# Kernel tuning notes

Hardware: AMD Instinct MI355X
Metric: run time of the kernel (lower is better)

## Reference

```python
import jax, jax.numpy as jnp
import numpy as np

EPS = 1e-5
K = 5          # kernel size from SE3Convolution(5, ...)
STRIDE = 2
PAD = 3
C_HID = 52     # 4*dim(repr3x3=9) + dim(repr7=7) + dim(repr9=9)
N_CLASSES = 10


def conv3d(x, w):
    # x: [N, Cin, D, H, W], w: [Cout, Cin, K, K, K]
    return jax.lax.conv_general_dilated(
        x, w,
        window_strides=(STRIDE, STRIDE, STRIDE),
        padding=[(PAD, PAD)] * 3,
        dimension_numbers=("NCDHW", "OIDHW", "NCDHW"),
    )


def bn3d(x):
    # training-mode batch norm over (batch, spatial), per channel, no affine
    mean = jnp.mean(x, axis=(0, 2, 3, 4), keepdims=True)
    var = jnp.var(x, axis=(0, 2, 3, 4), keepdims=True)
    return (x - mean) * jax.lax.rsqrt(var + EPS)


def setup_inputs() -> dict:
    key = jax.random.key(0)
    ks = jax.random.split(key, 10)
    x = jax.random.normal(ks[0], (32, 1, 64, 64, 64), dtype=jnp.float32)
    s = 0.05
    w0 = jax.random.normal(ks[1], (C_HID, 1, K, K, K), jnp.float32) * s
    b0 = jax.random.normal(ks[2], (C_HID,), jnp.float32) * s
    w1 = jax.random.normal(ks[3], (C_HID, C_HID, K, K, K), jnp.float32) * s
    b1 = jax.random.normal(ks[4], (C_HID,), jnp.float32) * s
    w2 = jax.random.normal(ks[5], (C_HID, C_HID, K, K, K), jnp.float32) * s
    b2 = jax.random.normal(ks[6], (C_HID,), jnp.float32) * s
    w3 = jax.random.normal(ks[7], (N_CLASSES, C_HID, K, K, K), jnp.float32) * s
    gamma = jnp.ones((N_CLASSES,), jnp.float32)
    beta = jnp.zeros((N_CLASSES,), jnp.float32)
    return {"x": x, "w0": w0, "b0": b0, "w1": w1, "b1": b1,
            "w2": w2, "b2": b2, "w3": w3, "gamma": gamma, "beta": beta}


def reference(x, w0, b0, w1, b1, w2, b2, w3, gamma, beta):
    # bn_in: BatchNorm3d(1, affine=False)
    h = bn3d(x)
    # three conv blocks with scalar batch norm + bias + ReLU (non_lin layers)
    for w, b in ((w0, b0), (w1, b1), (w2, b2)):
        h = conv3d(h, w)
        h = bn3d(h)
        h = jax.nn.relu(h + b[None, :, None, None, None])
    # final conv (no nonlinearity)
    h = conv3d(h, w3)
    # global average pool over x, y, z -> [batch, classes]
    h = jnp.mean(h, axis=(2, 3, 4))
    # bn_out: affine batch norm over the batch dim, per class
    mean = jnp.mean(h, axis=0, keepdims=True)
    var = jnp.var(h, axis=0, keepdims=True)
    h = (h - mean) * jax.lax.rsqrt(var + EPS)
    return h * gamma[None, :] + beta[None, :]
```

## Files before the change

kernel.cpp:

```cpp
#include <hip/hip_runtime.h>
#include <hip/hip_bf16.h>

#define EPSV 1e-5f
constexpr int NB = 32;

typedef short bf16x8 __attribute__((ext_vector_type(8)));
typedef short short4v __attribute__((ext_vector_type(4)));
typedef float f32x4 __attribute__((ext_vector_type(4)));

__device__ inline float bf2f(short s) {
  return __uint_as_float(((unsigned)(unsigned short)s) << 16);
}
__device__ inline short f2bf(float f) {
  unsigned u = __float_as_uint(f);
  unsigned r = (u + 0x7FFFu + ((u >> 16) & 1u)) >> 16;
  return (short)r;
}

__global__ __launch_bounds__(256) void reduce_partial_f32(
    const float* __restrict__ in, int spatial, float* __restrict__ part,
    int totb, int boff)
{
  const int b = blockIdx.x;
  const int nblk = gridDim.x;
  float s = 0.f, s2 = 0.f;
  for (int n = 0; n < NB; ++n) {
    const float* p = in + (size_t)n * spatial;
    for (int i = b * 256 + threadIdx.x; i < spatial; i += nblk * 256) {
      float v = p[i];
      s += v; s2 += v * v;
    }
  }
  __shared__ float sh[256], sh2[256];
  int tid = threadIdx.x;
  sh[tid] = s; sh2[tid] = s2;
  __syncthreads();
  for (int off = 128; off > 0; off >>= 1) {
    if (tid < off) { sh[tid] += sh[tid + off]; sh2[tid] += sh2[tid + off]; }
    __syncthreads();
  }
  if (tid == 0) {
    part[(size_t)(boff + b) * 2 + 0] = sh[0];
    part[(size_t)(boff + b) * 2 + 1] = sh2[0];
  }
}

__global__ __launch_bounds__(256) void reduce_cl(
    const short* __restrict__ y, long nrows,
    float* __restrict__ part, int totb, int boff)
{
  const int b = blockIdx.x, nblk = gridDim.x;
  const int c = threadIdx.x & 63, seg = threadIdx.x >> 6;
  float s = 0.f, s2 = 0.f;
  for (long r = (long)b * 4 + seg; r < nrows; r += (long)nblk * 4) {
    float v = bf2f(y[r * 64 + c]);
    s += v; s2 += v * v;
  }
  __shared__ float sh[4][64], sh2[4][64];
  sh[seg][c] = s; sh2[seg][c] = s2;
  __syncthreads();
  if (seg == 0) {
    float a = sh[0][c] + sh[1][c] + sh[2][c] + sh[3][c];
    float a2 = sh2[0][c] + sh2[1][c] + sh2[2][c] + sh2[3][c];
    part[((size_t)c * totb + boff + b) * 2 + 0] = a;
    part[((size_t)c * totb + boff + b) * 2 + 1] = a2;
  }
}

__global__ __launch_bounds__(64) void reduce_final(
    const float* __restrict__ part, int nblk, int C, float* __restrict__ sums)
{
  const int c = blockIdx.x;
  float s = 0.f, s2 = 0.f;
  for (int b = threadIdx.x; b < nblk; b += 64) {
    s  += part[((size_t)c * nblk + b) * 2 + 0];
    s2 += part[((size_t)c * nblk + b) * 2 + 1];
  }
  for (int off = 32; off > 0; off >>= 1) {
    s  += __shfl_down(s, off);
    s2 += __shfl_down(s2, off);
  }
  if (threadIdx.x == 0) { sums[c] = s; sums[C + c] = s2; }
}

__global__ __launch_bounds__(64) void aff_k(
    const float* __restrict__ st, const float* __restrict__ bias,
    float cnt_inv, int creal, float* __restrict__ a, float* __restrict__ c)
{
  int t = threadIdx.x;
  float mean = st[t] * cnt_inv;
  float var  = st[64 + t] * cnt_inv - mean * mean;
  float inv  = rsqrtf(var + EPSV);
  bool ok = t < creal;
  a[t] = ok ? inv : 0.f;
  c[t] = ok ? (-mean * inv + bias[t]) : 0.f;
}

__global__ __launch_bounds__(256) void repack_k(
    const float* __restrict__ w, short* __restrict__ wt,
    int CO, int CIN, int COP)
{
  long total = 125L * COP * 64;
  for (long idx = (long)blockIdx.x * 256 + threadIdx.x; idx < total;
       idx += (long)gridDim.x * 256) {
    int tap = (int)(idx / (COP * 64));
    int r   = (int)(idx % (COP * 64));
    int co = r >> 6, ci = r & 63;
    float v = (co < CO && ci < CIN) ? w[((size_t)co * CIN + ci) * 125 + tap] : 0.f;
    wt[idx] = f2bf(v);
  }
}

__global__ __launch_bounds__(256) void repack_w0(
    const float* __restrict__ w, short* __restrict__ wt)
{
  for (int idx = blockIdx.x * 256 + threadIdx.x; idx < 64 * 128;
       idx += gridDim.x * 256) {
    int co = idx >> 7, k = idx & 127;
    float v = (co < 52 && k < 125) ? w[co * 125 + k] : 0.f;
    wt[idx] = f2bf(v);
  }
}

__global__ __launch_bounds__(256) void conv0_mfma(
    const float* __restrict__ x, const short* __restrict__ w0t,
    const float* __restrict__ stats, short* __restrict__ out,
    int n_in0, int n_out0)
{
  constexpr int IN = 64, OUT = 33;
  constexpr float CNTI = 1.0f / ((float)NB * IN * IN * IN);
  __shared__ __align__(16) char slab[64 * 256];

  const int tid = threadIdx.x;
  const int wv = tid >> 6, ln = tid & 63;
  const int cs = ln >> 4;
  const int ntile0 = blockIdx.x * 64;
  const int od = blockIdx.y;
  const int img = blockIdx.z;

  const float mean = stats[0] * CNTI;
  const float inv  = rsqrtf(stats[1] * CNTI - mean * mean + EPSV);

  bf16x8 afr[4];
  {
    const short* wrow = w0t + (wv * 16 + (ln & 15)) * 128 + cs * 8;
    #pragma unroll
    for (int ks = 0; ks < 4; ++ks) afr[ks] = *(const bf16x8*)(wrow + ks * 32);
  }

  const float* xi = x + (size_t)(n_in0 + img) * (IN * IN * IN);
  const int id_base = 2 * od - 3;
  for (int u = tid; u < 1024; u += 256) {
    const int nl = u >> 4, s = u & 15;
    const int ng = ntile0 + nl;
    const int oh = ng / OUT, ow = ng - oh * OUT;
    const bool nok = ng < OUT * OUT;
    const int ih_base = 2 * oh - 3, iw_base = 2 * ow - 3;
    bf16x8 pk;
    #pragma unroll
    for (int e = 0; e < 8; ++e) {
      const int k = s * 8 + e;
      float f = 0.f;
      if (nok && k < 125) {
        const int kd = k / 25, r = k - kd * 25;
        const int kh = r / 5, kw = r - kh * 5;
        const int id = id_base + kd, ih = ih_base + kh, iw = iw_base + kw;
        if ((unsigned)id < (unsigned)IN && (unsigned)ih < (unsigned)IN &&
            (unsigned)iw < (unsigned)IN)
          f = (xi[((size_t)id * IN + ih) * IN + iw] - mean) * inv;
      }
      pk[e] = f2bf(f);
    }
    const int slot = (s & 8) | ((s & 7) ^ (nl & 7));
    *(bf16x8*)(slab + nl * 256 + slot * 16) = pk;
  }
  __syncthreads();

  const int nl = ln & 15;
  #pragma unroll
  for (int nt = 0; nt < 4; ++nt) {
    f32x4 acc = (f32x4){0.f, 0.f, 0.f, 0.f};
    const int nn = nt * 16 + nl;
    #pragma unroll
    for (int ks = 0; ks < 4; ++ks) {
      const int s = ks * 4 + cs;
      const int slot = (s & 8) | ((s & 7) ^ (nn & 7));
      bf16x8 b = *(const bf16x8*)(slab + nn * 256 + slot * 16);
      acc = __builtin_amdgcn_mfma_f32_16x16x32_bf16(afr[ks], b, acc, 0, 0, 0);
    }
    const int ng = ntile0 + nn;
    if (ng < OUT * OUT) {
      const int oh = ng / OUT, ow = ng - oh * OUT;
      short4v pk;
      #pragma unroll
      for (int r = 0; r < 4; ++r) pk[r] = f2bf(acc[r]);
      size_t base = ((((size_t)(n_out0 + img) * OUT + od) * OUT + oh) * OUT + ow) * 64;
      *(short4v*)(out + base + wv * 16 + cs * 4) = pk;
    }
  }
}

__device__ inline int swz(int lin, int cs) {
  int row = lin >> 1;
  int slot = (((lin & 1) << 2) | cs) ^ (row & 7);
  return row * 128 + slot * 16;
}

__device__ __forceinline__ void loada2(bf16x8 (&dst)[2][5], const short* __restrict__ wt,
                                       int tapb, int ch, int wm, int nl, int cs) {
  #pragma unroll
  for (int mi = 0; mi < 2; ++mi)
    #pragma unroll
    for (int kw = 0; kw < 5; ++kw)
      dst[mi][kw] = *(const bf16x8*)(
          wt + ((size_t)(tapb + kw) * 64 + (2 * wm + mi) * 16 + nl) * 64 + ch * 32 + cs * 8);
}

template<int IN, int OUT, int OHG>
__global__ __launch_bounds__(256, 2) void conv_2m2n(
    const short* __restrict__ yin, const short* __restrict__ wt,
    const float* __restrict__ affa, const float* __restrict__ affc,
    short* __restrict__ yout, int n_out0)
{
  constexpr int W = 2 * OUT + 3;
  constexpr int H = 2 * OHG + 3;
  constexpr int LIN = H * W;
  constexpr int ROWS = (LIN + 1) / 2;
  constexpr int OHT = (OUT + OHG - 1) / OHG;
  constexpr int LINM = LIN - 1 - 4 * W - 4;

  __shared__ __align__(16) char slab[ROWS * 128];
  __shared__ float s_a[64], s_c[64];

  const int tid = threadIdx.x;
  const int wv = tid >> 6, ln = tid & 63;
  const int nl = ln & 15, cs = ln >> 4;
  const int wm = wv >> 1, wn = wv & 1;

  int lin;
  if (gridDim.x & 7) lin = blockIdx.x;
  else {
    const int q = gridDim.x >> 3;
    lin = (blockIdx.x & 7) * q + (blockIdx.x >> 3);
  }
  const int oht = lin % OHT;
  const int t2  = lin / OHT;
  const int od  = t2 % OUT;
  const int nimg = t2 / OUT;
  const int oh0 = oht * OHG;

  if (tid < 64) { s_a[tid] = affa[tid]; s_c[tid] = affc[tid]; }

  int lb[2]; bool vld[2]; size_t obase[2];
  #pragma unroll
  for (int j = 0; j < 2; ++j) {
    int nt = 2 * wn + j;
    int n = nt * 16 + nl;
    int ohl = n / OUT, ow = n - ohl * OUT;
    vld[j] = n < OHG * OUT;
    int l = 2 * ohl * W + 2 * ow;
    lb[j] = (l > LINM) ? LINM : l;
    obase[j] = ((((size_t)(n_out0 + nimg) * OUT + od) * OUT + (oh0 + ohl)) * OUT + ow) * 64;
  }

  f32x4 acc[2][2];
  #pragma unroll
  for (int mi = 0; mi < 2; ++mi)
    #pragma unroll
    for (int j = 0; j < 2; ++j) acc[mi][j] = (f32x4){0.f, 0.f, 0.f, 0.f};

  const int id_base = 2 * od - 3;
  const int ih_base = 2 * oh0 - 3;

  for (int ch = 0; ch < 2; ++ch) {
    for (int kd = 0; kd < 5; ++kd) {
      __syncthreads();
      {
        const int id = id_base + kd;
        const bool dok = (unsigned)id < (unsigned)IN;
        for (int u = tid; u < LIN * 4; u += 256) {
          int l = u >> 2, cs2 = u & 3;
          int hl = l / W, wl = l - hl * W;
          int ih = ih_base + hl;
          int iw = wl - 3;
          bf16x8 pk;
          if (dok && (unsigned)ih < (unsigned)IN && (unsigned)iw < (unsigned)IN) {
            size_t base = ((((size_t)nimg * IN + id) * IN + ih) * IN + iw) * 64
                          + ch * 32 + cs2 * 8;
            bf16x8 ld = *(const bf16x8*)(yin + base);
            #pragma unroll
            for (int e = 0; e < 8; ++e) {
              int c = ch * 32 + cs2 * 8 + e;
              pk[e] = f2bf(fmaxf(s_a[c] * bf2f(ld[e]) + s_c[c], 0.f));
            }
          } else {
            #pragma unroll
            for (int e = 0; e < 8; ++e) pk[e] = 0;
          }
          *(bf16x8*)(slab + swz(l, cs2)) = pk;
        }
      }
      bf16x8 afr[2][2][5];
      loada2(afr[0], wt, (kd * 5 + 0) * 5, ch, wm, nl, cs);
      __builtin_amdgcn_sched_barrier(0);
      __syncthreads();
      #pragma unroll
      for (int kh = 0; kh < 5; ++kh) {
        if (kh < 4)
          loada2(afr[(kh + 1) & 1], wt, (kd * 5 + kh + 1) * 5, ch, wm, nl, cs);
        __builtin_amdgcn_sched_barrier(0);
        #pragma unroll
        for (int kw = 0; kw < 5; ++kw) {
          bf16x8 b0 = *(const bf16x8*)(slab + swz(lb[0] + kh * W + kw, cs));
          bf16x8 b1 = *(const bf16x8*)(slab + swz(lb[1] + kh * W + kw, cs));
          #pragma unroll
          for (int mi = 0; mi < 2; ++mi) {
            acc[mi][0] = __builtin_amdgcn_mfma_f32_16x16x32_bf16(
                afr[kh & 1][mi][kw], b0, acc[mi][0], 0, 0, 0);
            acc[mi][1] = __builtin_amdgcn_mfma_f32_16x16x32_bf16(
                afr[kh & 1][mi][kw], b1, acc[mi][1], 0, 0, 0);
          }
        }
      }
    }
  }

  #pragma unroll
  for (int j = 0; j < 2; ++j) {
    if (!vld[j]) continue;
    #pragma unroll
    for (int mi = 0; mi < 2; ++mi) {
      short4v pk;
      #pragma unroll
      for (int r = 0; r < 4; ++r) pk[r] = f2bf(acc[mi][j][r]);
      *(short4v*)(yout + obase[j] + (2 * wm + mi) * 16 + cs * 4) = pk;
    }
  }
}

__global__ __launch_bounds__(256) void conv3_m(
    const short* __restrict__ yin, const short* __restrict__ wt,
    const float* __restrict__ affa, const float* __restrict__ affc,
    short* __restrict__ yout)
{
  constexpr int IN = 10, OUT = 6;
  constexpr int W = 15, LIN = 225, ROWS = 113;
  constexpr int LINM = LIN - 1 - 4 * W - 4;
  __shared__ __align__(16) char slab[ROWS * 128];
  __shared__ float s_a[64], s_c[64];

  const int tid = threadIdx.x, wv = tid >> 6, ln = tid & 63;
  const int nl = ln & 15, cs = ln >> 4;
  const int od = blockIdx.x, nimg = blockIdx.y;

  if (tid < 64) { s_a[tid] = affa[tid]; s_c[tid] = affc[tid]; }

  const int nn = wv * 16 + nl;
  const bool act = wv < 3;
  const bool vld = act && nn < 36;
  int ohl = nn / 6, ow = nn - ohl * 6;
  int lb = 2 * ohl * W + 2 * ow;
  if (lb > LINM) lb = LINM;
  const size_t obase = ((((size_t)nimg * 6 + od) * 6 + ohl) * 6 + ow) * 16;

  f32x4 acc = (f32x4){0.f, 0.f, 0.f, 0.f};
  const int id_base = 2 * od - 3;

  for (int ch = 0; ch < 2; ++ch) {
    for (int kd = 0; kd < 5; ++kd) {
      const int id = id_base + kd;
      const bool dok = (unsigned)id < (unsigned)IN;
      __syncthreads();
      for (int u = tid; u < 900; u += 256) {
        int l = u >> 2, cs2 = u & 3;
        int hl = l / 15, wl = l - hl * 15;
        int ih = hl - 3, iw = wl - 3;
        bf16x8 pk;
        if (dok && (unsigned)ih < (unsigned)IN && (unsigned)iw < (unsigned)IN) {
          bf16x8 ld = *(const bf16x8*)(yin + ((((size_t)nimg * IN + id) * IN + ih) * IN + iw) * 64
                                       + ch * 32 + cs2 * 8);
          #pragma unroll
          for (int e = 0; e < 8; ++e) {
            int c = ch * 32 + cs2 * 8 + e;
            pk[e] = f2bf(fmaxf(s_a[c] * bf2f(ld[e]) + s_c[c], 0.f));
          }
        } else {
          #pragma unroll
          for (int e = 0; e < 8; ++e) pk[e] = 0;
        }
        *(bf16x8*)(slab + swz(l, cs2)) = pk;
      }
      __syncthreads();
      if (act) {
        for (int kh = 0; kh < 5; ++kh) {
          const int tapb = (kd * 5 + kh) * 5;
          bf16x8 afr[5];
          #pragma unroll
          for (int kw = 0; kw < 5; ++kw)
            afr[kw] = *(const bf16x8*)(wt + ((size_t)(tapb + kw) * 16 + nl) * 64
                                       + ch * 32 + cs * 8);
          #pragma unroll
          for (int kw = 0; kw < 5; ++kw) {
            bf16x8 b = *(const bf16x8*)(slab + swz(lb + kh * W + kw, cs));
            acc = __builtin_amdgcn_mfma_f32_16x16x32_bf16(afr[kw], b, acc, 0, 0, 0);
          }
        }
      }
    }
  }
  if (vld) {
    short4v pk;
    #pragma unroll
    for (int r = 0; r < 4; ++r) pk[r] = f2bf(acc[r]);
    *(short4v*)(yout + obase + cs * 4) = pk;
  }
}

__global__ __launch_bounds__(320) void pool_bn(
    const short* __restrict__ y3, const float* __restrict__ gamma,
    const float* __restrict__ beta, float* __restrict__ out)
{
  __shared__ float pool[320];
  const int t = threadIdx.x;
  const int n = t / 10, c = t % 10;
  const short* p = y3 + (size_t)n * 216 * 16 + c;
  float s = 0.f;
  for (int i = 0; i < 216; ++i) s += bf2f(p[i * 16]);
  const float pv = s * (1.0f / 216.0f);
  pool[t] = pv;
  __syncthreads();
  float m = 0.f, m2 = 0.f;
  for (int nn = 0; nn < 32; ++nn) {
    float v = pool[nn * 10 + c];
    m += v; m2 += v * v;
  }
  m *= (1.0f / 32.0f);
  m2 = m2 * (1.0f / 32.0f) - m * m;
  out[t] = (pv - m) * rsqrtf(m2 + EPSV) * gamma[c] + beta[c];
}

extern "C" void kernel_launch(void* const* d_in, const int* in_sizes, int n_in,
                              void* d_out, int out_size, void* d_ws, size_t ws_size,
                              hipStream_t stream)
{
  const float* x  = (const float*)d_in[0];
  const float* w0 = (const float*)d_in[1];
  const float* b0 = (const float*)d_in[2];
  const float* w1 = (const float*)d_in[3];
  const float* b1 = (const float*)d_in[4];
  const float* w2 = (const float*)d_in[5];
  const float* b2 = (const float*)d_in[6];
  const float* w3 = (const float*)d_in[7];
  const float* gamma = (const float*)d_in[8];
  const float* beta  = (const float*)d_in[9];
  float* out = (float*)d_out;

  char* base = (char*)d_ws;
  size_t off = 0;
  auto alloc = [&](size_t bytes) -> void* {
    void* p = base + off;
    off = (off + bytes + 255) & ~(size_t)255;
    return p;
  };
  short* y1  = (short*)alloc((size_t)32 * 5832 * 64 * 2);
  short* y2  = (short*)alloc((size_t)32 * 1000 * 64 * 2);
  short* y3  = (short*)alloc((size_t)32 * 216 * 16 * 2);
  short* w1t = (short*)alloc((size_t)125 * 64 * 64 * 2);
  short* w2t = (short*)alloc((size_t)125 * 64 * 64 * 2);
  short* w3t = (short*)alloc((size_t)125 * 16 * 64 * 2);
  short* w0t = (short*)alloc((size_t)64 * 128 * 2);
  float* st_in = (float*)alloc(1024);
  float* st0 = (float*)alloc(1024);
  float* st1 = (float*)alloc(1024);
  float* st2 = (float*)alloc(1024);
  float* a0 = (float*)alloc(256); float* c0 = (float*)alloc(256);
  float* a1 = (float*)alloc(256); float* c1 = (float*)alloc(256);
  float* a2 = (float*)alloc(256); float* c2 = (float*)alloc(256);
  float* part = (float*)alloc(64 * 1024 * 2 * 4);
  short* y0 = (short*)(base + off);
  size_t rem = (ws_size > off + 256) ? (ws_size - off - 256) : 0;
  const size_t Y0_IMG = (size_t)35937 * 64;
  int CH;
  if      (rem >= Y0_IMG * 32 * 2) CH = 32;
  else if (rem >= Y0_IMG * 16 * 2) CH = 16;
  else if (rem >= Y0_IMG * 8 * 2)  CH = 8;
  else if (rem >= Y0_IMG * 4 * 2)  CH = 4;
  else if (rem >= Y0_IMG * 2 * 2)  CH = 2;
  else                             CH = 1;
  const int nch = 32 / CH;

  repack_k<<<512, 256, 0, stream>>>(w1, w1t, 52, 52, 64);
  repack_k<<<512, 256, 0, stream>>>(w2, w2t, 52, 52, 64);
  repack_k<<<256, 256, 0, stream>>>(w3, w3t, 10, 52, 16);
  repack_w0<<<32, 256, 0, stream>>>(w0, w0t);

  reduce_partial_f32<<<128, 256, 0, stream>>>(x, 64 * 64 * 64, part, 128, 0);
  reduce_final<<<1, 64, 0, stream>>>(part, 128, 1, st_in);

  const float cnt0 = 1.0f / ((float)NB * 35937.0f);
  const float cnt1 = 1.0f / ((float)NB * 5832.0f);
  const float cnt2 = 1.0f / ((float)NB * 1000.0f);

  if (CH == 32) {
    conv0_mfma<<<dim3(18, 33, 32), 256, 0, stream>>>(x, w0t, st_in, y0, 0, 0);
    reduce_cl<<<1024, 256, 0, stream>>>(y0, (long)32 * 35937, part, 1024, 0);
    reduce_final<<<64, 64, 0, stream>>>(part, 1024, 64, st0);
    aff_k<<<1, 64, 0, stream>>>(st0, b0, cnt0, 52, a0, c0);
    conv_2m2n<33, 18, 3><<<6 * 18 * 32, 256, 0, stream>>>(
        y0, w1t, a0, c0, y1, 0);
  } else {
    for (int ck = 0; ck < nch; ++ck) {
      conv0_mfma<<<dim3(18, 33, CH), 256, 0, stream>>>(x, w0t, st_in, y0, ck * CH, 0);
      reduce_cl<<<32, 256, 0, stream>>>(y0, (long)CH * 35937, part, nch * 32, ck * 32);
    }
    reduce_final<<<64, 64, 0, stream>>>(part, nch * 32, 64, st0);
    aff_k<<<1, 64, 0, stream>>>(st0, b0, cnt0, 52, a0, c0);
    for (int ck = 0; ck < nch; ++ck) {
      conv0_mfma<<<dim3(18, 33, CH), 256, 0, stream>>>(x, w0t, st_in, y0, ck * CH, 0);
      conv_2m2n<33, 18, 3><<<6 * 18 * CH, 256, 0, stream>>>(
          y0, w1t, a0, c0, y1, ck * CH);
    }
  }

  reduce_cl<<<256, 256, 0, stream>>>(y1, (long)32 * 5832, part, 256, 0);
  reduce_final<<<64, 64, 0, stream>>>(part, 256, 64, st1);
  aff_k<<<1, 64, 0, stream>>>(st1, b1, cnt1, 52, a1, c1);

  conv_2m2n<18, 10, 5><<<2 * 10 * 32, 256, 0, stream>>>(
      y1, w2t, a1, c1, y2, 0);

  reduce_cl<<<32, 256, 0, stream>>>(y2, (long)32 * 1000, part, 32, 0);
  reduce_final<<<64, 64, 0, stream>>>(part, 32, 64, st2);
  aff_k<<<1, 64, 0, stream>>>(st2, b2, cnt2, 52, a2, c2);

  conv3_m<<<dim3(6, 32), 256, 0, stream>>>(y2, w3t, a2, c2, y3);

  pool_bn<<<1, 320, 0, stream>>>(y3, gamma, beta, out);
}
```

Baseline: 1.589 ms.

## Restructure conv kernel so each wave owns one M tile over all N tiles

The conv kernel changes from a 2x2 split of output channels and spatial tiles across waves to one where each wave owns 16 output channels and loops over every N tile. The row-group size shrinks (3 to 2 for conv1, 5 to 4 for conv2), so the grid grows, and the double-buffered weight prefetch with scheduling barriers goes away in favour of a plain per-kh load. A bounds check on the output height is added for the partial last tile. This raises the number of LDS B-fragment reads per MFMA and drops the occupancy hint of 2, in exchange for fewer weight registers and simpler code.

```diff
diff --git a/kernel.cpp b/kernel.cpp
--- a/kernel.cpp
+++ b/kernel.cpp
@@ -206,18 +206,8 @@
   return row * 128 + slot * 16;
 }
 
-__device__ __forceinline__ void loada2(bf16x8 (&dst)[2][5], const short* __restrict__ wt,
-                                       int tapb, int ch, int wm, int nl, int cs) {
-  #pragma unroll
-  for (int mi = 0; mi < 2; ++mi)
-    #pragma unroll
-    for (int kw = 0; kw < 5; ++kw)
-      dst[mi][kw] = *(const bf16x8*)(
-          wt + ((size_t)(tapb + kw) * 64 + (2 * wm + mi) * 16 + nl) * 64 + ch * 32 + cs * 8);
-}
-
 template<int IN, int OUT, int OHG>
-__global__ __launch_bounds__(256, 2) void conv_2m2n(
+__global__ __launch_bounds__(256) void conv_m4(
     const short* __restrict__ yin, const short* __restrict__ wt,
     const float* __restrict__ affa, const float* __restrict__ affc,
     short* __restrict__ yout, int n_out0)
@@ -226,6 +216,7 @@
   constexpr int H = 2 * OHG + 3;
   constexpr int LIN = H * W;
   constexpr int ROWS = (LIN + 1) / 2;
+  constexpr int NT = (OHG * OUT + 15) / 16;
   constexpr int OHT = (OUT + OHG - 1) / OHG;
   constexpr int LINM = LIN - 1 - 4 * W - 4;
 
@@ -235,7 +226,6 @@
   const int tid = threadIdx.x;
   const int wv = tid >> 6, ln = tid & 63;
   const int nl = ln & 15, cs = ln >> 4;
-  const int wm = wv >> 1, wn = wv & 1;
 
   int lin;
   if (gridDim.x & 7) lin = blockIdx.x;
@@ -251,23 +241,20 @@
 
   if (tid < 64) { s_a[tid] = affa[tid]; s_c[tid] = affc[tid]; }
 
-  int lb[2]; bool vld[2]; size_t obase[2];
+  int lb[NT]; bool vld[NT]; size_t obase[NT];
   #pragma unroll
-  for (int j = 0; j < 2; ++j) {
-    int nt = 2 * wn + j;
+  for (int nt = 0; nt < NT; ++nt) {
     int n = nt * 16 + nl;
     int ohl = n / OUT, ow = n - ohl * OUT;
-    vld[j] = n < OHG * OUT;
+    vld[nt] = (n < OHG * OUT) && (oh0 + ohl < OUT);
     int l = 2 * ohl * W + 2 * ow;
-    lb[j] = (l > LINM) ? LINM : l;
-    obase[j] = ((((size_t)(n_out0 + nimg) * OUT + od) * OUT + (oh0 + ohl)) * OUT + ow) * 64;
-  }
-
-  f32x4 acc[2][2];
+    lb[nt] = (l > LINM) ? LINM : l;
+    obase[nt] = ((((size_t)(n_out0 + nimg) * OUT + od) * OUT + (oh0 + ohl)) * OUT + ow) * 64;
+  }
+
+  f32x4 acc[NT];
   #pragma unroll
-  for (int mi = 0; mi < 2; ++mi)
-    #pragma unroll
-    for (int j = 0; j < 2; ++j) acc[mi][j] = (f32x4){0.f, 0.f, 0.f, 0.f};
+  for (int nt = 0; nt < NT; ++nt) acc[nt] = (f32x4){0.f, 0.f, 0.f, 0.f};
 
   const int id_base = 2 * od - 3;
   const int ih_base = 2 * oh0 - 3;
@@ -300,25 +287,22 @@
           *(bf16x8*)(slab + swz(l, cs2)) = pk;
         }
       }
-      bf16x8 afr[2][2][5];
-      loada2(afr[0], wt, (kd * 5 + 0) * 5, ch, wm, nl, cs);
-      __builtin_amdgcn_sched_barrier(0);
       __syncthreads();
-      #pragma unroll
       for (int kh = 0; kh < 5; ++kh) {
-        if (kh < 4)
-          loada2(afr[(kh + 1) & 1], wt, (kd * 5 + kh + 1) * 5, ch, wm, nl, cs);
-        __builtin_amdgcn_sched_barrier(0);
+        const int tapb = (kd * 5 + kh) * 5;
+        bf16x8 afr[5];
         #pragma unroll
-        for (int kw = 0; kw < 5; ++kw) {
-          bf16x8 b0 = *(const bf16x8*)(slab + swz(lb[0] + kh * W + kw, cs));
-          bf16x8 b1 = *(const bf16x8*)(slab + swz(lb[1] + kh * W + kw, cs));
+        for (int kw = 0; kw < 5; ++kw)
+          afr[kw] = *(const bf16x8*)(
+              wt + ((size_t)(tapb + kw) * 64 + wv * 16 + nl) * 64 + ch * 32 + cs * 8);
+        #pragma unroll
+        for (int nt = 0; nt < NT; ++nt) {
+          const int lin0 = lb[nt] + kh * W;
           #pragma unroll
-          for (int mi = 0; mi < 2; ++mi) {
-            acc[mi][0] = __builtin_amdgcn_mfma_f32_16x16x32_bf16(
-                afr[kh & 1][mi][kw], b0, acc[mi][0], 0, 0, 0);
-            acc[mi][1] = __builtin_amdgcn_mfma_f32_16x16x32_bf16(
-                afr[kh & 1][mi][kw], b1, acc[mi][1], 0, 0, 0);
+          for (int kw = 0; kw < 5; ++kw) {
+            bf16x8 b = *(const bf16x8*)(slab + swz(lin0 + kw, cs));
+            acc[nt] = __builtin_amdgcn_mfma_f32_16x16x32_bf16(
+                afr[kw], b, acc[nt], 0, 0, 0);
           }
         }
       }
@@ -326,15 +310,12 @@
   }
 
   #pragma unroll
-  for (int j = 0; j < 2; ++j) {
-    if (!vld[j]) continue;
+  for (int nt = 0; nt < NT; ++nt) {
+    if (!vld[nt]) continue;
+    short4v pk;
     #pragma unroll
-    for (int mi = 0; mi < 2; ++mi) {
-      short4v pk;
-      #pragma unroll
-      for (int r = 0; r < 4; ++r) pk[r] = f2bf(acc[mi][j][r]);
-      *(short4v*)(yout + obase[j] + (2 * wm + mi) * 16 + cs * 4) = pk;
-    }
+    for (int r = 0; r < 4; ++r) pk[r] = f2bf(acc[nt][r]);
+    *(short4v*)(yout + obase[nt] + wv * 16 + cs * 4) = pk;
   }
 }
 
@@ -506,7 +487,7 @@
     reduce_cl<<<1024, 256, 0, stream>>>(y0, (long)32 * 35937, part, 1024, 0);
     reduce_final<<<64, 64, 0, stream>>>(part, 1024, 64, st0);
     aff_k<<<1, 64, 0, stream>>>(st0, b0, cnt0, 52, a0, c0);
-    conv_2m2n<33, 18, 3><<<6 * 18 * 32, 256, 0, stream>>>(
+    conv_m4<33, 18, 2><<<9 * 18 * 32, 256, 0, stream>>>(
         y0, w1t, a0, c0, y1, 0);
   } else {
     for (int ck = 0; ck < nch; ++ck) {
@@ -517,7 +498,7 @@
     aff_k<<<1, 64, 0, stream>>>(st0, b0, cnt0, 52, a0, c0);
     for (int ck = 0; ck < nch; ++ck) {
       conv0_mfma<<<dim3(18, 33, CH), 256, 0, stream>>>(x, w0t, st_in, y0, ck * CH, 0);
-      conv_2m2n<33, 18, 3><<<6 * 18 * CH, 256, 0, stream>>>(
+      conv_m4<33, 18, 2><<<9 * 18 * CH, 256, 0, stream>>>(
           y0, w1t, a0, c0, y1, ck * CH);
     }
   }
@@ -526,7 +507,7 @@
   reduce_final<<<64, 64, 0, stream>>>(part, 256, 64, st1);
   aff_k<<<1, 64, 0, stream>>>(st1, b1, cnt1, 52, a1, c1);
 
-  conv_2m2n<18, 10, 5><<<2 * 10 * 32, 256, 0, stream>>>(
+  conv_m4<18, 10, 4><<<3 * 10 * 32, 256, 0, stream>>>(
       y1, w2t, a1, c1, y2, 0);
 
   reduce_cl<<<32, 256, 0, stream>>>(y2, (long)32 * 1000, part, 32, 0);
```

Measured after the change: 1.304 ms, median of 3. 17.9% less time.
